# Kernel tuning notes

Hardware: AMD Instinct MI355X
Metric: run time of the kernel (lower is better)

Reference implementation:

```python
import jax, jax.numpy as jnp
import numpy as np

D = 1024

def setup_inputs() -> dict:
    key = jax.random.key(0)
    k1, k2, k3, k4, k5 = jax.random.split(key, 5)
    B, S = 128, 512
    seq_output = jax.random.normal(k1, (B, S, D), dtype=jnp.float32)
    mask = jax.random.randint(k2, (B, S), 0, 2) == 1  # True = masked position
    # ensure last position is never fully-masked pathological: fine either way
    scale1 = 1.0 / np.sqrt(D)
    W1 = jax.random.normal(k3, (D, D), dtype=jnp.float32) * scale1
    b1 = jnp.zeros((D,), dtype=jnp.float32)
    w2 = jax.random.normal(k4, (D,), dtype=jnp.float32) * scale1
    return {"seq_output": seq_output, "mask": mask, "W1": W1, "b1": b1, "w2": w2}

def reference(seq_output, mask, W1, b1, w2):
    # u_last: last timestep embedding
    u_last = seq_output[:, -1, :]                           # [B, D]
    # additive attention MLP: Linear -> tanh -> Linear(D->1, no bias)
    h = jnp.tanh(jnp.einsum('bsd,de->bse', seq_output, W1) + b1)  # [B, S, D]
    scores = jnp.einsum('bsd,d->bs', h, w2)                 # [B, S]
    scores = jnp.where(mask, -1e9, scores)
    attn = jax.nn.softmax(scores, axis=-1)                  # [B, S]
    u_att = jnp.einsum('bs,bsd->bd', attn, seq_output)      # [B, D]
    return (u_last, u_att)
```

## Files before the change

### kernel.cpp

```cpp
#include <hip/hip_runtime.h>
#include <hip/hip_bf16.h>
#include <cstdint>
#include <cstddef>

#define BATCH 128
#define SEQ   512
#define DIM   1024
#define MROWS (BATCH * SEQ)
#define NT    32

typedef short short8 __attribute__((ext_vector_type(8)));
typedef __bf16 bf16x8 __attribute__((ext_vector_type(8)));
typedef float f32x4 __attribute__((ext_vector_type(4)));

template <typename VA> struct other_frag { using type = bf16x8; };
template <> struct other_frag<bf16x8> { using type = short8; };

template <typename VA>
__device__ __forceinline__ auto try_mfma(VA a, VA b, f32x4 c, int)
    -> decltype(__builtin_amdgcn_mfma_f32_16x16x32_bf16(a, b, c, 0, 0, 0)) {
  return __builtin_amdgcn_mfma_f32_16x16x32_bf16(a, b, c, 0, 0, 0);
}
template <typename VA>
__device__ __forceinline__ f32x4 try_mfma(VA a, VA b, f32x4 c, long) {
  using O = typename other_frag<VA>::type;
  O a2 = __builtin_bit_cast(O, a);
  O b2 = __builtin_bit_cast(O, b);
  return __builtin_amdgcn_mfma_f32_16x16x32_bf16(a2, b2, c, 0, 0, 0);
}
__device__ __forceinline__ f32x4 mfma_bf16(short8 a, short8 b, f32x4 c) {
  return try_mfma(a, b, c, 0);
}

__device__ __forceinline__ unsigned short f32_to_bf16(float f) {
  union { float f; uint32_t u; } v; v.f = f;
  uint32_t u = v.u;
  u += 0x7FFFu + ((u >> 16) & 1u);
  return (unsigned short)(u >> 16);
}

__device__ __forceinline__ float bf16_to_f32(unsigned short u) {
  union { uint32_t u; float f; } v; v.u = ((uint32_t)u) << 16; return v.f;
}

__device__ __forceinline__ void gload_lds16(const void* g, void* l) {
  __builtin_amdgcn_global_load_lds(
      (__attribute__((address_space(1))) void*)g,
      (__attribute__((address_space(3))) void*)l,
      16, 0, 0);
}

__device__ __forceinline__ float fast_tanh(float x) {
  x = fminf(fmaxf(x, -15.0f), 15.0f);
  float e = __expf(2.0f * x);
  return (e - 1.0f) / (e + 1.0f);
}

__global__ __launch_bounds__(256) void cast_x_kernel(const float* __restrict__ X,
                                                     unsigned short* __restrict__ Xb) {
  const int total8 = MROWS * DIM / 8;
  int idx = blockIdx.x * 256 + threadIdx.x;
  const int stride = 2048 * 256;
  for (int i = idx; i < total8; i += stride) {
    const f32x4* p = (const f32x4*)X + (size_t)i * 2;
    f32x4 a = p[0];
    f32x4 b = p[1];
    short8 o;
    o[0] = (short)f32_to_bf16(a[0]); o[1] = (short)f32_to_bf16(a[1]);
    o[2] = (short)f32_to_bf16(a[2]); o[3] = (short)f32_to_bf16(a[3]);
    o[4] = (short)f32_to_bf16(b[0]); o[5] = (short)f32_to_bf16(b[1]);
    o[6] = (short)f32_to_bf16(b[2]); o[7] = (short)f32_to_bf16(b[3]);
    *((short8*)Xb + i) = o;
  }
}

__global__ __launch_bounds__(256) void w1t_kernel(const float* __restrict__ W1,
                                                  unsigned short* __restrict__ W1t) {
  __shared__ float tile[64][65];
  int bx = blockIdx.x & 15;
  int by = blockIdx.x >> 4;
  int t = threadIdx.x;
  int c = t & 63, r0 = t >> 6;
#pragma unroll
  for (int i = 0; i < 16; i++) {
    int r = i * 4 + r0;
    tile[r][c] = W1[(size_t)(by * 64 + r) * DIM + bx * 64 + c];
  }
  __syncthreads();
#pragma unroll
  for (int i = 0; i < 16; i++) {
    int r = i * 4 + r0;
    W1t[(size_t)(bx * 64 + r) * DIM + by * 64 + c] = f32_to_bf16(tile[c][r]);
  }
}

__global__ __launch_bounds__(256) void ulast_kernel(const float* __restrict__ X,
                                                    float* __restrict__ u_last) {
  int i = blockIdx.x * 256 + threadIdx.x;
  int b = i >> 8;
  int d4 = i & 255;
  ((f32x4*)u_last)[i] = ((const f32x4*)X)[((size_t)b * SEQ + (SEQ - 1)) * 256 + d4];
}

__global__ __launch_bounds__(512, 2) void gemm_score_kernel(
    const unsigned short* __restrict__ Xb,
    const unsigned short* __restrict__ W1t,
    const float* __restrict__ b1,
    const float* __restrict__ w2,
    float* __restrict__ scores) {
  __shared__ __align__(16) char lds[131072];

  const int tid = threadIdx.x;
  const int lane = tid & 63;
  const int w = tid >> 6;
  const int wr = w >> 2, wc = w & 3;

  const int bx = blockIdx.x;
  const int swz = (bx & 7) * 128 + (bx >> 3);
  const int m0 = (swz >> 2) * 256;
  const int n0 = (swz & 3) * 256;

  const unsigned short *a0Src, *a1Src, *b0Src, *b1Src;
  {
    int sc0 = w * 64 + lane;
    int sr0 = sc0 >> 3, j0 = (sc0 & 7) ^ (sr0 & 7);
    int row0 = sr0 * 2 + (j0 >> 2), c40 = j0 & 3;
    a0Src = Xb  + (size_t)(m0 + row0) * DIM + c40 * 8;
    b0Src = W1t + (size_t)(n0 + row0) * DIM + c40 * 8;
    int sc1 = (8 + w) * 64 + lane;
    int sr1 = sc1 >> 3, j1 = (sc1 & 7) ^ (sr1 & 7);
    int row1 = sr1 * 2 + (j1 >> 2), c41 = j1 & 3;
    a1Src = Xb  + (size_t)(m0 + row1) * DIM + c41 * 8;
    b1Src = W1t + (size_t)(n0 + row1) * DIM + c41 * 8;
  }
  const int dst0 = w * 1024;
  const int dst1 = (8 + w) * 1024;

  int aOff[8];
#pragma unroll
  for (int mi = 0; mi < 8; mi++) {
    int row = wr * 128 + mi * 16 + (lane & 15);
    int srow = row >> 1;
    int ic = ((row & 1) * 4 + (lane >> 4)) ^ (srow & 7);
    aOff[mi] = srow * 128 + ic * 16;
  }
  int bOff[4];
#pragma unroll
  for (int ni = 0; ni < 4; ni++) {
    int row = wc * 64 + ni * 16 + (lane & 15);
    int srow = row >> 1;
    int ic = ((row & 1) * 4 + (lane >> 4)) ^ (srow & 7);
    bOff[ni] = 65536 + srow * 128 + ic * 16;
  }

  f32x4 acc[8][4];
#pragma unroll
  for (int mi = 0; mi < 8; mi++)
#pragma unroll
    for (int ni = 0; ni < 4; ni++)
      acc[mi][ni] = (f32x4){0.f, 0.f, 0.f, 0.f};

#define STAGE(S) do {                                                   \
    const int bufS_ = ((S) & 3) * 16384;                                \
    const int ktS_ = (S) * 32;                                          \
    gload_lds16(a0Src + ktS_, lds + bufS_ + dst0);                      \
    gload_lds16(a1Src + ktS_, lds + bufS_ + dst1);                      \
    gload_lds16(b0Src + ktS_, lds + 65536 + bufS_ + dst0);              \
    gload_lds16(b1Src + ktS_, lds + 65536 + bufS_ + dst1);              \
  } while (0)

#define KITER(S, VMSTR) do {                                            \
    asm volatile("s_waitcnt vmcnt(" VMSTR ")" ::: "memory");            \
    __builtin_amdgcn_s_barrier();                                       \
    __builtin_amdgcn_sched_barrier(0);                                  \
    if ((S) + 3 < NT) STAGE((S) + 3);                                   \
    const int buf_ = ((S) & 3) * 16384;                                 \
    short8 af[8], bfv[4];                                               \
    _Pragma("unroll")                                                   \
    for (int mi = 0; mi < 8; mi++)                                      \
      af[mi] = *(const short8*)(lds + buf_ + aOff[mi]);                 \
    _Pragma("unroll")                                                   \
    for (int ni = 0; ni < 4; ni++)                                      \
      bfv[ni] = *(const short8*)(lds + buf_ + bOff[ni]);                \
    __builtin_amdgcn_s_setprio(1);                                      \
    _Pragma("unroll")                                                   \
    for (int mi = 0; mi < 8; mi++)                                      \
      _Pragma("unroll")                                                 \
      for (int ni = 0; ni < 4; ni++)                                    \
        acc[mi][ni] = mfma_bf16(af[mi], bfv[ni], acc[mi][ni]);          \
    __builtin_amdgcn_s_setprio(0);                                      \
  } while (0)

  STAGE(0); STAGE(1); STAGE(2);

  for (int s = 0; s < NT - 2; ++s) KITER(s, "8");
  KITER(NT - 2, "4");
  KITER(NT - 1, "0");

#undef STAGE
#undef KITER

  const int cg = lane >> 4;
  const int cl = lane & 15;
#pragma unroll
  for (int mi = 0; mi < 8; mi++) {
    float p0 = 0.f, p1 = 0.f, p2 = 0.f, p3 = 0.f;
#pragma unroll
    for (int ni = 0; ni < 4; ni++) {
      int col = n0 + wc * 64 + ni * 16 + cl;
      float w2v = w2[col];
      float b1v = b1[col];
      p0 += fast_tanh(acc[mi][ni][0] + b1v) * w2v;
      p1 += fast_tanh(acc[mi][ni][1] + b1v) * w2v;
      p2 += fast_tanh(acc[mi][ni][2] + b1v) * w2v;
      p3 += fast_tanh(acc[mi][ni][3] + b1v) * w2v;
    }
#pragma unroll
    for (int off = 1; off < 16; off <<= 1) {
      p0 += __shfl_xor(p0, off);
      p1 += __shfl_xor(p1, off);
      p2 += __shfl_xor(p2, off);
      p3 += __shfl_xor(p3, off);
    }
    if (cl == 0) {
      int row = m0 + wr * 128 + mi * 16 + cg * 4;
      atomicAdd(&scores[row + 0], p0);
      atomicAdd(&scores[row + 1], p1);
      atomicAdd(&scores[row + 2], p2);
      atomicAdd(&scores[row + 3], p3);
    }
  }
}

__global__ __launch_bounds__(256) void attn_uatt_kernel(
    const unsigned short* __restrict__ Xb,
    const float* __restrict__ scores,
    const int* __restrict__ mask,
    float* __restrict__ u_att) {
  const int b = blockIdx.x;
  const int half = blockIdx.y;
  const int tid = threadIdx.x;
  const int lane = tid & 63;
  const int wave = tid >> 6;

  __shared__ float attn[SEQ];
  __shared__ float rbuf[4];
  __shared__ float part[3][64 * 9];

  float s0 = scores[(size_t)b * SEQ + tid];
  float s1 = scores[(size_t)b * SEQ + 256 + tid];
  if (mask[(size_t)b * SEQ + tid]) s0 = -1000000000.0f;
  if (mask[(size_t)b * SEQ + 256 + tid]) s1 = -1000000000.0f;

  float mx = fmaxf(s0, s1);
#pragma unroll
  for (int off = 1; off < 64; off <<= 1) mx = fmaxf(mx, __shfl_xor(mx, off));
  if (lane == 0) rbuf[wave] = mx;
  __syncthreads();
  mx = fmaxf(fmaxf(rbuf[0], rbuf[1]), fmaxf(rbuf[2], rbuf[3]));

  float p0 = expf(s0 - mx), p1 = expf(s1 - mx);
  float sm = p0 + p1;
#pragma unroll
  for (int off = 1; off < 64; off <<= 1) sm += __shfl_xor(sm, off);
  __syncthreads();
  if (lane == 0) rbuf[wave] = sm;
  __syncthreads();
  sm = rbuf[0] + rbuf[1] + rbuf[2] + rbuf[3];
  float inv = 1.0f / sm;
  attn[tid] = p0 * inv;
  attn[tid + 256] = p1 * inv;
  __syncthreads();

  const int col = tid & 63;
  const int sh = tid >> 6;
  const short8* Xp = (const short8*)Xb + (size_t)b * SEQ * (DIM / 8) + half * 64 + col;
  float a[8] = {0.f, 0.f, 0.f, 0.f, 0.f, 0.f, 0.f, 0.f};
  for (int s = sh * 128; s < sh * 128 + 128; s++) {
    short8 v = Xp[(size_t)s * (DIM / 8)];
    float wgt = attn[s];
#pragma unroll
    for (int j = 0; j < 8; j++)
      a[j] += wgt * bf16_to_f32((unsigned short)v[j]);
  }
  if (sh) {
#pragma unroll
    for (int j = 0; j < 8; j++) part[sh - 1][col * 9 + j] = a[j];
  }
  __syncthreads();
  if (sh == 0) {
#pragma unroll
    for (int j = 0; j < 8; j++)
      a[j] += part[0][col * 9 + j] + part[1][col * 9 + j] + part[2][col * 9 + j];
    f32x4 lo = {a[0], a[1], a[2], a[3]};
    f32x4 hi = {a[4], a[5], a[6], a[7]};
    f32x4* dst = (f32x4*)(u_att + (size_t)b * DIM + half * 512 + col * 8);
    dst[0] = lo;
    dst[1] = hi;
  }
}

extern "C" void kernel_launch(void* const* d_in, const int* in_sizes, int n_in,
                              void* d_out, int out_size, void* d_ws, size_t ws_size,
                              hipStream_t stream) {
  const float* X    = (const float*)d_in[0];
  const int*   mask = (const int*)d_in[1];
  const float* W1   = (const float*)d_in[2];
  const float* b1   = (const float*)d_in[3];
  const float* w2   = (const float*)d_in[4];

  float* out    = (float*)d_out;
  float* u_last = out;
  float* u_att  = out + BATCH * DIM;

  char* ws = (char*)d_ws;
  unsigned short* Xb  = (unsigned short*)ws;
  unsigned short* W1t = (unsigned short*)(ws + (size_t)MROWS * DIM * 2);
  float* scores = (float*)(ws + (size_t)MROWS * DIM * 2 + (size_t)DIM * DIM * 2);

  hipMemsetAsync(scores, 0, MROWS * sizeof(float), stream);
  hipLaunchKernelGGL(cast_x_kernel, dim3(2048), dim3(256), 0, stream, X, Xb);
  hipLaunchKernelGGL(w1t_kernel, dim3(256), dim3(256), 0, stream, W1, W1t);
  hipLaunchKernelGGL(ulast_kernel, dim3(128), dim3(256), 0, stream, X, u_last);
  hipLaunchKernelGGL(gemm_score_kernel, dim3(1024), dim3(512), 0, stream,
                     Xb, W1t, b1, w2, scores);
  hipLaunchKernelGGL(attn_uatt_kernel, dim3(128, 2), dim3(256), 0, stream,
                     Xb, scores, mask, u_att);
}
```

Baseline: 266.6 us.

## Fuse fp32-to-bf16 cast of X into GEMM A-tile loading and drop cast kernel

The separate cast kernel that wrote a bf16 copy of X is removed. The GEMM now loads fp32 A tiles into registers, packs them to bf16 and writes them to LDS through a restructured double-buffered pipeline, with B going to a triple buffer and each K step split into two half-M MFMA phases. The attention kernel reads fp32 X directly and also writes u_last, which drops the ulast kernel. This removes a full write and re-read of the 128 MB bf16 copy, but the GEMM now reads twice as many A bytes (fp32) per tile, repeated across the four N-tile blocks, and adds more barriers per iteration.

```diff
diff --git a/kernel.cpp b/kernel.cpp
--- a/kernel.cpp
+++ b/kernel.cpp
@@ -39,8 +39,13 @@
   return (unsigned short)(u >> 16);
 }
 
-__device__ __forceinline__ float bf16_to_f32(unsigned short u) {
-  union { uint32_t u; float f; } v; v.u = ((uint32_t)u) << 16; return v.f;
+__device__ __forceinline__ short8 pack8(f32x4 a, f32x4 b) {
+  short8 o;
+  o[0] = (short)f32_to_bf16(a[0]); o[1] = (short)f32_to_bf16(a[1]);
+  o[2] = (short)f32_to_bf16(a[2]); o[3] = (short)f32_to_bf16(a[3]);
+  o[4] = (short)f32_to_bf16(b[0]); o[5] = (short)f32_to_bf16(b[1]);
+  o[6] = (short)f32_to_bf16(b[2]); o[7] = (short)f32_to_bf16(b[3]);
+  return o;
 }
 
 __device__ __forceinline__ void gload_lds16(const void* g, void* l) {
@@ -54,24 +59,6 @@
   x = fminf(fmaxf(x, -15.0f), 15.0f);
   float e = __expf(2.0f * x);
   return (e - 1.0f) / (e + 1.0f);
-}
-
-__global__ __launch_bounds__(256) void cast_x_kernel(const float* __restrict__ X,
-                                                     unsigned short* __restrict__ Xb) {
-  const int total8 = MROWS * DIM / 8;
-  int idx = blockIdx.x * 256 + threadIdx.x;
-  const int stride = 2048 * 256;
-  for (int i = idx; i < total8; i += stride) {
-    const f32x4* p = (const f32x4*)X + (size_t)i * 2;
-    f32x4 a = p[0];
-    f32x4 b = p[1];
-    short8 o;
-    o[0] = (short)f32_to_bf16(a[0]); o[1] = (short)f32_to_bf16(a[1]);
-    o[2] = (short)f32_to_bf16(a[2]); o[3] = (short)f32_to_bf16(a[3]);
-    o[4] = (short)f32_to_bf16(b[0]); o[5] = (short)f32_to_bf16(b[1]);
-    o[6] = (short)f32_to_bf16(b[2]); o[7] = (short)f32_to_bf16(b[3]);
-    *((short8*)Xb + i) = o;
-  }
 }
 
 __global__ __launch_bounds__(256) void w1t_kernel(const float* __restrict__ W1,
@@ -94,21 +81,13 @@
   }
 }
 
-__global__ __launch_bounds__(256) void ulast_kernel(const float* __restrict__ X,
-                                                    float* __restrict__ u_last) {
-  int i = blockIdx.x * 256 + threadIdx.x;
-  int b = i >> 8;
-  int d4 = i & 255;
-  ((f32x4*)u_last)[i] = ((const f32x4*)X)[((size_t)b * SEQ + (SEQ - 1)) * 256 + d4];
-}
-
 __global__ __launch_bounds__(512, 2) void gemm_score_kernel(
-    const unsigned short* __restrict__ Xb,
+    const float* __restrict__ Xf,
     const unsigned short* __restrict__ W1t,
     const float* __restrict__ b1,
     const float* __restrict__ w2,
     float* __restrict__ scores) {
-  __shared__ __align__(16) char lds[131072];
+  __shared__ __align__(16) char lds[81920];
 
   const int tid = threadIdx.x;
   const int lane = tid & 63;
@@ -120,37 +99,36 @@
   const int m0 = (swz >> 2) * 256;
   const int n0 = (swz & 3) * 256;
 
-  const unsigned short *a0Src, *a1Src, *b0Src, *b1Src;
+  const int j_sw = (tid & 7) ^ ((tid >> 3) & 7);
+  const int ar0 = (tid >> 3) * 2 + (j_sw >> 2);
+  const float* aS0 = Xf + (size_t)(m0 + ar0) * DIM + (j_sw & 3) * 8;
+
+  const unsigned short *b0Src, *b1Src;
   {
-    int sc0 = w * 64 + lane;
-    int sr0 = sc0 >> 3, j0 = (sc0 & 7) ^ (sr0 & 7);
+    int sr0 = tid >> 3, j0 = (tid & 7) ^ (sr0 & 7);
     int row0 = sr0 * 2 + (j0 >> 2), c40 = j0 & 3;
-    a0Src = Xb  + (size_t)(m0 + row0) * DIM + c40 * 8;
     b0Src = W1t + (size_t)(n0 + row0) * DIM + c40 * 8;
-    int sc1 = (8 + w) * 64 + lane;
+    int sc1 = 512 + tid;
     int sr1 = sc1 >> 3, j1 = (sc1 & 7) ^ (sr1 & 7);
     int row1 = sr1 * 2 + (j1 >> 2), c41 = j1 & 3;
-    a1Src = Xb  + (size_t)(m0 + row1) * DIM + c41 * 8;
     b1Src = W1t + (size_t)(n0 + row1) * DIM + c41 * 8;
   }
-  const int dst0 = w * 1024;
-  const int dst1 = (8 + w) * 1024;
-
-  int aOff[8];
-#pragma unroll
-  for (int mi = 0; mi < 8; mi++) {
+
+  int aOffL[4];
+#pragma unroll
+  for (int mi = 0; mi < 4; mi++) {
     int row = wr * 128 + mi * 16 + (lane & 15);
-    int srow = row >> 1;
-    int ic = ((row & 1) * 4 + (lane >> 4)) ^ (srow & 7);
-    aOff[mi] = srow * 128 + ic * 16;
-  }
-  int bOff[4];
+    int sr = row >> 1;
+    int j = ((row & 1) * 4 + (lane >> 4)) ^ (sr & 7);
+    aOffL[mi] = sr * 128 + j * 16;
+  }
+  int bOffL[4];
 #pragma unroll
   for (int ni = 0; ni < 4; ni++) {
     int row = wc * 64 + ni * 16 + (lane & 15);
-    int srow = row >> 1;
-    int ic = ((row & 1) * 4 + (lane >> 4)) ^ (srow & 7);
-    bOff[ni] = 65536 + srow * 128 + ic * 16;
+    int sr = row >> 1;
+    int j = ((row & 1) * 4 + (lane >> 4)) ^ (sr & 7);
+    bOffL[ni] = sr * 128 + j * 16;
   }
 
   f32x4 acc[8][4];
@@ -160,45 +138,113 @@
     for (int ni = 0; ni < 4; ni++)
       acc[mi][ni] = (f32x4){0.f, 0.f, 0.f, 0.f};
 
-#define STAGE(S) do {                                                   \
-    const int bufS_ = ((S) & 3) * 16384;                                \
-    const int ktS_ = (S) * 32;                                          \
-    gload_lds16(a0Src + ktS_, lds + bufS_ + dst0);                      \
-    gload_lds16(a1Src + ktS_, lds + bufS_ + dst1);                      \
-    gload_lds16(b0Src + ktS_, lds + 65536 + bufS_ + dst0);              \
-    gload_lds16(b1Src + ktS_, lds + 65536 + bufS_ + dst1);              \
+  f32x4 rA0[4], rA1[4];
+  short8 af[4], bf[4];
+
+#define LOAD_A(SET, T) do {                                              \
+    const float* aP_ = aS0 + (T) * 32;                                   \
+    SET[0] = *(const f32x4*)(aP_);                                       \
+    SET[1] = *(const f32x4*)(aP_ + 4);                                   \
+    SET[2] = *(const f32x4*)(aP_ + (size_t)128 * DIM);                   \
+    SET[3] = *(const f32x4*)(aP_ + (size_t)128 * DIM + 4);               \
   } while (0)
 
-#define KITER(S, VMSTR) do {                                            \
-    asm volatile("s_waitcnt vmcnt(" VMSTR ")" ::: "memory");            \
-    __builtin_amdgcn_s_barrier();                                       \
-    __builtin_amdgcn_sched_barrier(0);                                  \
-    if ((S) + 3 < NT) STAGE((S) + 3);                                   \
-    const int buf_ = ((S) & 3) * 16384;                                 \
-    short8 af[8], bfv[4];                                               \
-    _Pragma("unroll")                                                   \
-    for (int mi = 0; mi < 8; mi++)                                      \
-      af[mi] = *(const short8*)(lds + buf_ + aOff[mi]);                 \
-    _Pragma("unroll")                                                   \
-    for (int ni = 0; ni < 4; ni++)                                      \
-      bfv[ni] = *(const short8*)(lds + buf_ + bOff[ni]);                \
-    __builtin_amdgcn_s_setprio(1);                                      \
-    _Pragma("unroll")                                                   \
-    for (int mi = 0; mi < 8; mi++)                                      \
-      _Pragma("unroll")                                                 \
-      for (int ni = 0; ni < 4; ni++)                                    \
-        acc[mi][ni] = mfma_bf16(af[mi], bfv[ni], acc[mi][ni]);          \
-    __builtin_amdgcn_s_setprio(0);                                      \
+  LOAD_A(rA0, 0);
+  __builtin_amdgcn_sched_barrier(0);
+  gload_lds16(b0Src, lds + 32768 + w * 1024);
+  gload_lds16(b1Src, lds + 32768 + 8192 + w * 1024);
+  __builtin_amdgcn_sched_barrier(0);
+  LOAD_A(rA1, 1);
+  __builtin_amdgcn_sched_barrier(0);
+  gload_lds16(b0Src + 32, lds + 32768 + 16384 + w * 1024);
+  gload_lds16(b1Src + 32, lds + 32768 + 16384 + 8192 + w * 1024);
+  __builtin_amdgcn_sched_barrier(0);
+  asm volatile("s_waitcnt vmcnt(8)" ::: "memory");
+  {
+    short8 w0 = pack8(rA0[0], rA0[1]);
+    short8 w1 = pack8(rA0[2], rA0[3]);
+    char* wd = lds + tid * 16;
+    *(short8*)wd = w0;
+    *(short8*)(wd + 8192) = w1;
+  }
+  asm volatile("s_waitcnt vmcnt(6)" ::: "memory");
+  asm volatile("s_waitcnt lgkmcnt(0)" ::: "memory");
+  __builtin_amdgcn_sched_barrier(0);
+  __builtin_amdgcn_s_barrier();
+
+#define BODY(S, ISET, WSET, PF, DOWR, VMSTR) do {                        \
+                                               \
+    if (PF) {                                                            \
+      LOAD_A(ISET, (S) + 2);                                             \
+      gload_lds16(b0Src + ((S) + 2) * 32,                                \
+                  lds + 32768 + (((S) + 2) % 3) * 16384 + w * 1024);     \
+    }                                                                    \
+    __builtin_amdgcn_sched_barrier(0);                                   \
+    {                                                                    \
+      const char* bA_ = lds + ((S) & 1) * 16384;                         \
+      const char* bB_ = lds + 32768 + ((S) % 3) * 16384;                 \
+      af[0] = *(const short8*)(bA_ + aOffL[0]);                          \
+      af[1] = *(const short8*)(bA_ + aOffL[1]);                          \
+      af[2] = *(const short8*)(bA_ + aOffL[2]);                          \
+      af[3] = *(const short8*)(bA_ + aOffL[3]);                          \
+      bf[0] = *(const short8*)(bB_ + bOffL[0]);                          \
+      bf[1] = *(const short8*)(bB_ + bOffL[1]);                          \
+      bf[2] = *(const short8*)(bB_ + bOffL[2]);                          \
+      bf[3] = *(const short8*)(bB_ + bOffL[3]);                          \
+    }                                                                    \
+    __builtin_amdgcn_sched_barrier(0);                                   \
+    __builtin_amdgcn_s_barrier();                                        \
+    __builtin_amdgcn_s_setprio(1);                                       \
+    _Pragma("unroll")                                                    \
+    for (int mi = 0; mi < 4; mi++)                                       \
+      _Pragma("unroll")                                                  \
+      for (int ni = 0; ni < 4; ni++)                                     \
+        acc[mi][ni] = mfma_bf16(af[mi], bf[ni], acc[mi][ni]);            \
+    __builtin_amdgcn_s_setprio(0);                                       \
+    __builtin_amdgcn_s_barrier();                                        \
+                                               \
+    asm volatile("s_waitcnt vmcnt(" VMSTR ")" ::: "memory");             \
+    __builtin_amdgcn_sched_barrier(0);                                   \
+    if (DOWR) {                                                          \
+      short8 w0_ = pack8(WSET[0], WSET[1]);                              \
+      short8 w1_ = pack8(WSET[2], WSET[3]);                              \
+      char* wd_ = lds + (((S) + 1) & 1) * 16384 + tid * 16;              \
+      *(short8*)wd_ = w0_;                                               \
+      *(short8*)(wd_ + 8192) = w1_;                                      \
+    }                                                                    \
+    if (PF)                                                              \
+      gload_lds16(b1Src + ((S) + 2) * 32,                                \
+                  lds + 32768 + (((S) + 2) % 3) * 16384 + 8192 + w * 1024); \
+    __builtin_amdgcn_sched_barrier(0);                                   \
+    {                                                                    \
+      const char* bA_ = lds + ((S) & 1) * 16384;                         \
+      af[0] = *(const short8*)(bA_ + aOffL[0] + 4096);                   \
+      af[1] = *(const short8*)(bA_ + aOffL[1] + 4096);                   \
+      af[2] = *(const short8*)(bA_ + aOffL[2] + 4096);                   \
+      af[3] = *(const short8*)(bA_ + aOffL[3] + 4096);                   \
+    }                                                                    \
+    __builtin_amdgcn_sched_barrier(0);                                   \
+    __builtin_amdgcn_s_barrier();                                        \
+    __builtin_amdgcn_s_setprio(1);                                       \
+    _Pragma("unroll")                                                    \
+    for (int mi = 0; mi < 4; mi++)                                       \
+      _Pragma("unroll")                                                  \
+      for (int ni = 0; ni < 4; ni++)                                     \
+        acc[mi + 4][ni] = mfma_bf16(af[mi], bf[ni], acc[mi + 4][ni]);    \
+    __builtin_amdgcn_s_setprio(0);                                       \
+    __builtin_amdgcn_s_barrier();                                        \
   } while (0)
 
-  STAGE(0); STAGE(1); STAGE(2);
-
-  for (int s = 0; s < NT - 2; ++s) KITER(s, "8");
-  KITER(NT - 2, "4");
-  KITER(NT - 1, "0");
-
-#undef STAGE
-#undef KITER
+  for (int t = 0; t < 15; ++t) {
+    const int S0 = 2 * t;
+    BODY(S0, rA0, rA1, 1, 1, "5");
+    BODY(S0 + 1, rA1, rA0, 1, 1, "5");
+  }
+  BODY(30, rA0, rA1, 0, 1, "0");
+  BODY(31, rA1, rA0, 0, 0, "0");
+
+#undef BODY
+#undef LOAD_A
 
   const int cg = lane >> 4;
   const int cl = lane & 15;
@@ -233,10 +279,11 @@
 }
 
 __global__ __launch_bounds__(256) void attn_uatt_kernel(
-    const unsigned short* __restrict__ Xb,
+    const float* __restrict__ X,
     const float* __restrict__ scores,
     const int* __restrict__ mask,
-    float* __restrict__ u_att) {
+    float* __restrict__ u_att,
+    float* __restrict__ u_last) {
   const int b = blockIdx.x;
   const int half = blockIdx.y;
   const int tid = threadIdx.x;
@@ -272,31 +319,37 @@
   attn[tid + 256] = p1 * inv;
   __syncthreads();
 
+  if (tid < 128) {
+    ((f32x4*)u_last)[(size_t)b * 256 + half * 128 + tid] =
+        ((const f32x4*)X)[((size_t)b * SEQ + (SEQ - 1)) * 256 + half * 128 + tid];
+  }
+
   const int col = tid & 63;
   const int sh = tid >> 6;
-  const short8* Xp = (const short8*)Xb + (size_t)b * SEQ * (DIM / 8) + half * 64 + col;
-  float a[8] = {0.f, 0.f, 0.f, 0.f, 0.f, 0.f, 0.f, 0.f};
+  const f32x4* Xp = (const f32x4*)X + (size_t)b * SEQ * 256 + half * 128 + col * 2;
+  f32x4 a0 = {0.f, 0.f, 0.f, 0.f}, a1 = {0.f, 0.f, 0.f, 0.f};
   for (int s = sh * 128; s < sh * 128 + 128; s++) {
-    short8 v = Xp[(size_t)s * (DIM / 8)];
     float wgt = attn[s];
-#pragma unroll
-    for (int j = 0; j < 8; j++)
-      a[j] += wgt * bf16_to_f32((unsigned short)v[j]);
+    a0 += wgt * Xp[(size_t)s * 256];
+    a1 += wgt * Xp[(size_t)s * 256 + 1];
   }
   if (sh) {
 #pragma unroll
-    for (int j = 0; j < 8; j++) part[sh - 1][col * 9 + j] = a[j];
+    for (int j = 0; j < 4; j++) part[sh - 1][col * 9 + j] = a0[j];
+#pragma unroll
+    for (int j = 0; j < 4; j++) part[sh - 1][col * 9 + 4 + j] = a1[j];
   }
   __syncthreads();
   if (sh == 0) {
 #pragma unroll
-    for (int j = 0; j < 8; j++)
-      a[j] += part[0][col * 9 + j] + part[1][col * 9 + j] + part[2][col * 9 + j];
-    f32x4 lo = {a[0], a[1], a[2], a[3]};
-    f32x4 hi = {a[4], a[5], a[6], a[7]};
+    for (int j = 0; j < 4; j++)
+      a0[j] += part[0][col * 9 + j] + part[1][col * 9 + j] + part[2][col * 9 + j];
+#pragma unroll
+    for (int j = 0; j < 4; j++)
+      a1[j] += part[0][col * 9 + 4 + j] + part[1][col * 9 + 4 + j] + part[2][col * 9 + 4 + j];
     f32x4* dst = (f32x4*)(u_att + (size_t)b * DIM + half * 512 + col * 8);
-    dst[0] = lo;
-    dst[1] = hi;
+    dst[0] = a0;
+    dst[1] = a1;
   }
 }
 
@@ -314,16 +367,13 @@
   float* u_att  = out + BATCH * DIM;
 
   char* ws = (char*)d_ws;
-  unsigned short* Xb  = (unsigned short*)ws;
-  unsigned short* W1t = (unsigned short*)(ws + (size_t)MROWS * DIM * 2);
-  float* scores = (float*)(ws + (size_t)MROWS * DIM * 2 + (size_t)DIM * DIM * 2);
+  unsigned short* W1t = (unsigned short*)ws;
+  float* scores = (float*)(ws + (size_t)DIM * DIM * 2);
 
   hipMemsetAsync(scores, 0, MROWS * sizeof(float), stream);
-  hipLaunchKernelGGL(cast_x_kernel, dim3(2048), dim3(256), 0, stream, X, Xb);
   hipLaunchKernelGGL(w1t_kernel, dim3(256), dim3(256), 0, stream, W1, W1t);
-  hipLaunchKernelGGL(ulast_kernel, dim3(128), dim3(256), 0, stream, X, u_last);
   hipLaunchKernelGGL(gemm_score_kernel, dim3(1024), dim3(512), 0, stream,
-                     Xb, W1t, b1, w2, scores);
+                     X, W1t, b1, w2, scores);
   hipLaunchKernelGGL(attn_uatt_kernel, dim3(128, 2), dim3(256), 0, stream,
-                     Xb, scores, mask, u_att);
-}
+                     X, scores, mask, u_att, u_last);
+}
```

New measurement: 256.0 us. -4.0%, faster.

## Split each K-iteration into two half-phases interleaving loads with MFMA

Applied to the files above, without the earlier changes.

Each K-step of the GEMM now runs in two phases. The first issues the A-tile global-to-LDS prefetch, reads half of the A fragments plus the B fragments, and runs half of the MFMAs. The second issues the B prefetch, reads the other half of A, and runs the remaining MFMAs. The aim is to cut fragment register pressure and spread memory issue across the MFMA work, ping-pong style. It adds three extra workgroup barriers per iteration, which could cost synchronisation time.

```diff
diff --git a/kernel.cpp b/kernel.cpp
--- a/kernel.cpp
+++ b/kernel.cpp
@@ -160,11 +160,18 @@
     for (int ni = 0; ni < 4; ni++)
       acc[mi][ni] = (f32x4){0.f, 0.f, 0.f, 0.f};
 
-#define STAGE(S) do {                                                   \
+  short8 af[4], bfv[4];
+
+#define STAGE_A(S) do {                                                 \
     const int bufS_ = ((S) & 3) * 16384;                                \
     const int ktS_ = (S) * 32;                                          \
     gload_lds16(a0Src + ktS_, lds + bufS_ + dst0);                      \
     gload_lds16(a1Src + ktS_, lds + bufS_ + dst1);                      \
+  } while (0)
+
+#define STAGE_B(S) do {                                                 \
+    const int bufS_ = ((S) & 3) * 16384;                                \
+    const int ktS_ = (S) * 32;                                          \
     gload_lds16(b0Src + ktS_, lds + 65536 + bufS_ + dst0);              \
     gload_lds16(b1Src + ktS_, lds + 65536 + bufS_ + dst1);              \
   } while (0)
@@ -173,31 +180,50 @@
     asm volatile("s_waitcnt vmcnt(" VMSTR ")" ::: "memory");            \
     __builtin_amdgcn_s_barrier();                                       \
     __builtin_amdgcn_sched_barrier(0);                                  \
-    if ((S) + 3 < NT) STAGE((S) + 3);                                   \
     const int buf_ = ((S) & 3) * 16384;                                 \
-    short8 af[8], bfv[4];                                               \
-    _Pragma("unroll")                                                   \
-    for (int mi = 0; mi < 8; mi++)                                      \
+                                                 \
+    if ((S) + 3 < NT) STAGE_A((S) + 3);                                 \
+    _Pragma("unroll")                                                   \
+    for (int mi = 0; mi < 4; mi++)                                      \
       af[mi] = *(const short8*)(lds + buf_ + aOff[mi]);                 \
     _Pragma("unroll")                                                   \
     for (int ni = 0; ni < 4; ni++)                                      \
       bfv[ni] = *(const short8*)(lds + buf_ + bOff[ni]);                \
+    __builtin_amdgcn_s_barrier();                                       \
     __builtin_amdgcn_s_setprio(1);                                      \
     _Pragma("unroll")                                                   \
-    for (int mi = 0; mi < 8; mi++)                                      \
+    for (int mi = 0; mi < 4; mi++)                                      \
       _Pragma("unroll")                                                 \
       for (int ni = 0; ni < 4; ni++)                                    \
         acc[mi][ni] = mfma_bf16(af[mi], bfv[ni], acc[mi][ni]);          \
     __builtin_amdgcn_s_setprio(0);                                      \
+    __builtin_amdgcn_s_barrier();                                       \
+    __builtin_amdgcn_sched_barrier(0);                                  \
+                                                 \
+    if ((S) + 3 < NT) STAGE_B((S) + 3);                                 \
+    _Pragma("unroll")                                                   \
+    for (int mi = 0; mi < 4; mi++)                                      \
+      af[mi] = *(const short8*)(lds + buf_ + aOff[mi + 4]);             \
+    __builtin_amdgcn_s_barrier();                                       \
+    __builtin_amdgcn_s_setprio(1);                                      \
+    _Pragma("unroll")                                                   \
+    for (int mi = 0; mi < 4; mi++)                                      \
+      _Pragma("unroll")                                                 \
+      for (int ni = 0; ni < 4; ni++)                                    \
+        acc[mi + 4][ni] = mfma_bf16(af[mi], bfv[ni], acc[mi + 4][ni]);  \
+    __builtin_amdgcn_s_setprio(0);                                      \
   } while (0)
 
-  STAGE(0); STAGE(1); STAGE(2);
+  STAGE_A(0); STAGE_B(0);
+  STAGE_A(1); STAGE_B(1);
+  STAGE_A(2); STAGE_B(2);
 
   for (int s = 0; s < NT - 2; ++s) KITER(s, "8");
   KITER(NT - 2, "4");
   KITER(NT - 1, "0");
 
-#undef STAGE
+#undef STAGE_A
+#undef STAGE_B
 #undef KITER
 
   const int cg = lane >> 4;
```

New measurement: 267.8 us. Within noise of the previous version (+0.5%).

## Switch GEMM to 32x32x16 MFMA tiles and fold u_last copy into cast kernel

Applied to the files above, without the earlier changes.

The main GEMM moves from 16x16x32 bf16 MFMA to 32x32x16 MFMA. LDS fragment offsets, the accumulator layout and the tanh/w2 epilogue reduction are reworked to match the 32x32 output layout. Each wave now issues fewer, larger MFMAs and fewer LDS fragment reads per K-step. The separate u_last gather kernel is removed, and the cast kernel writes the last-timestep rows while it converts X, saving one launch. The epilogue now does a wider shuffle reduction over 16 values per lane, which may raise register pressure.

```diff
diff --git a/kernel.cpp b/kernel.cpp
--- a/kernel.cpp
+++ b/kernel.cpp
@@ -12,24 +12,25 @@
 typedef short short8 __attribute__((ext_vector_type(8)));
 typedef __bf16 bf16x8 __attribute__((ext_vector_type(8)));
 typedef float f32x4 __attribute__((ext_vector_type(4)));
+typedef float f32x16 __attribute__((ext_vector_type(16)));
 
 template <typename VA> struct other_frag { using type = bf16x8; };
 template <> struct other_frag<bf16x8> { using type = short8; };
 
 template <typename VA>
-__device__ __forceinline__ auto try_mfma(VA a, VA b, f32x4 c, int)
-    -> decltype(__builtin_amdgcn_mfma_f32_16x16x32_bf16(a, b, c, 0, 0, 0)) {
-  return __builtin_amdgcn_mfma_f32_16x16x32_bf16(a, b, c, 0, 0, 0);
+__device__ __forceinline__ auto try_mfma32(VA a, VA b, f32x16 c, int)
+    -> decltype(__builtin_amdgcn_mfma_f32_32x32x16_bf16(a, b, c, 0, 0, 0)) {
+  return __builtin_amdgcn_mfma_f32_32x32x16_bf16(a, b, c, 0, 0, 0);
 }
 template <typename VA>
-__device__ __forceinline__ f32x4 try_mfma(VA a, VA b, f32x4 c, long) {
+__device__ __forceinline__ f32x16 try_mfma32(VA a, VA b, f32x16 c, long) {
   using O = typename other_frag<VA>::type;
   O a2 = __builtin_bit_cast(O, a);
   O b2 = __builtin_bit_cast(O, b);
-  return __builtin_amdgcn_mfma_f32_16x16x32_bf16(a2, b2, c, 0, 0, 0);
-}
-__device__ __forceinline__ f32x4 mfma_bf16(short8 a, short8 b, f32x4 c) {
-  return try_mfma(a, b, c, 0);
+  return __builtin_amdgcn_mfma_f32_32x32x16_bf16(a2, b2, c, 0, 0, 0);
+}
+__device__ __forceinline__ f32x16 mfma32_bf16(short8 a, short8 b, f32x16 c) {
+  return try_mfma32(a, b, c, 0);
 }
 
 __device__ __forceinline__ unsigned short f32_to_bf16(float f) {
@@ -57,7 +58,8 @@
 }
 
 __global__ __launch_bounds__(256) void cast_x_kernel(const float* __restrict__ X,
-                                                     unsigned short* __restrict__ Xb) {
+                                                     unsigned short* __restrict__ Xb,
+                                                     float* __restrict__ u_last) {
   const int total8 = MROWS * DIM / 8;
   int idx = blockIdx.x * 256 + threadIdx.x;
   const int stride = 2048 * 256;
@@ -71,6 +73,13 @@
     o[4] = (short)f32_to_bf16(b[0]); o[5] = (short)f32_to_bf16(b[1]);
     o[6] = (short)f32_to_bf16(b[2]); o[7] = (short)f32_to_bf16(b[3]);
     *((short8*)Xb + i) = o;
+    int row = i >> 7;
+    if ((row & (SEQ - 1)) == SEQ - 1) {
+      int g = i & 127;
+      f32x4* dst = (f32x4*)(u_last + (size_t)(row >> 9) * DIM + g * 8);
+      dst[0] = a;
+      dst[1] = b;
+    }
   }
 }
 
@@ -92,14 +101,6 @@
     int r = i * 4 + r0;
     W1t[(size_t)(bx * 64 + r) * DIM + by * 64 + c] = f32_to_bf16(tile[c][r]);
   }
-}
-
-__global__ __launch_bounds__(256) void ulast_kernel(const float* __restrict__ X,
-                                                    float* __restrict__ u_last) {
-  int i = blockIdx.x * 256 + threadIdx.x;
-  int b = i >> 8;
-  int d4 = i & 255;
-  ((f32x4*)u_last)[i] = ((const f32x4*)X)[((size_t)b * SEQ + (SEQ - 1)) * 256 + d4];
 }
 
 __global__ __launch_bounds__(512, 2) void gemm_score_kernel(
@@ -136,29 +137,37 @@
   const int dst0 = w * 1024;
   const int dst1 = (8 + w) * 1024;
 
-  int aOff[8];
-#pragma unroll
-  for (int mi = 0; mi < 8; mi++) {
-    int row = wr * 128 + mi * 16 + (lane & 15);
+  int aOff[4][2];
+#pragma unroll
+  for (int mi = 0; mi < 4; mi++) {
+    int row = wr * 128 + mi * 32 + (lane & 31);
     int srow = row >> 1;
-    int ic = ((row & 1) * 4 + (lane >> 4)) ^ (srow & 7);
-    aOff[mi] = srow * 128 + ic * 16;
-  }
-  int bOff[4];
-#pragma unroll
-  for (int ni = 0; ni < 4; ni++) {
-    int row = wc * 64 + ni * 16 + (lane & 15);
+#pragma unroll
+    for (int kk = 0; kk < 2; kk++) {
+      int ic = ((row & 1) * 4 + kk * 2 + (lane >> 5)) ^ (srow & 7);
+      aOff[mi][kk] = srow * 128 + ic * 16;
+    }
+  }
+  int bOff[2][2];
+#pragma unroll
+  for (int ni = 0; ni < 2; ni++) {
+    int row = wc * 64 + ni * 32 + (lane & 31);
     int srow = row >> 1;
-    int ic = ((row & 1) * 4 + (lane >> 4)) ^ (srow & 7);
-    bOff[ni] = 65536 + srow * 128 + ic * 16;
-  }
-
-  f32x4 acc[8][4];
-#pragma unroll
-  for (int mi = 0; mi < 8; mi++)
-#pragma unroll
-    for (int ni = 0; ni < 4; ni++)
-      acc[mi][ni] = (f32x4){0.f, 0.f, 0.f, 0.f};
+#pragma unroll
+    for (int kk = 0; kk < 2; kk++) {
+      int ic = ((row & 1) * 4 + kk * 2 + (lane >> 5)) ^ (srow & 7);
+      bOff[ni][kk] = 65536 + srow * 128 + ic * 16;
+    }
+  }
+
+  f32x16 acc[4][2];
+#pragma unroll
+  for (int mi = 0; mi < 4; mi++)
+#pragma unroll
+    for (int ni = 0; ni < 2; ni++)
+      acc[mi][ni] = (f32x16)(0.f);
+
+  short8 af[4][2], bfv[2][2];
 
 #define STAGE(S) do {                                                   \
     const int bufS_ = ((S) & 3) * 16384;                                \
@@ -175,19 +184,24 @@
     __builtin_amdgcn_sched_barrier(0);                                  \
     if ((S) + 3 < NT) STAGE((S) + 3);                                   \
     const int buf_ = ((S) & 3) * 16384;                                 \
-    short8 af[8], bfv[4];                                               \
     _Pragma("unroll")                                                   \
-    for (int mi = 0; mi < 8; mi++)                                      \
-      af[mi] = *(const short8*)(lds + buf_ + aOff[mi]);                 \
+    for (int mi = 0; mi < 4; mi++)                                      \
+      _Pragma("unroll")                                                 \
+      for (int kk = 0; kk < 2; kk++)                                    \
+        af[mi][kk] = *(const short8*)(lds + buf_ + aOff[mi][kk]);       \
     _Pragma("unroll")                                                   \
-    for (int ni = 0; ni < 4; ni++)                                      \
-      bfv[ni] = *(const short8*)(lds + buf_ + bOff[ni]);                \
+    for (int ni = 0; ni < 2; ni++)                                      \
+      _Pragma("unroll")                                                 \
+      for (int kk = 0; kk < 2; kk++)                                    \
+        bfv[ni][kk] = *(const short8*)(lds + buf_ + bOff[ni][kk]);      \
     __builtin_amdgcn_s_setprio(1);                                      \
     _Pragma("unroll")                                                   \
-    for (int mi = 0; mi < 8; mi++)                                      \
+    for (int kk = 0; kk < 2; kk++)                                      \
       _Pragma("unroll")                                                 \
-      for (int ni = 0; ni < 4; ni++)                                    \
-        acc[mi][ni] = mfma_bf16(af[mi], bfv[ni], acc[mi][ni]);          \
+      for (int mi = 0; mi < 4; mi++)                                    \
+        _Pragma("unroll")                                               \
+        for (int ni = 0; ni < 2; ni++)                                  \
+          acc[mi][ni] = mfma32_bf16(af[mi][kk], bfv[ni][kk], acc[mi][ni]); \
     __builtin_amdgcn_s_setprio(0);                                      \
   } while (0)
 
@@ -200,34 +214,35 @@
 #undef STAGE
 #undef KITER
 
-  const int cg = lane >> 4;
-  const int cl = lane & 15;
-#pragma unroll
-  for (int mi = 0; mi < 8; mi++) {
-    float p0 = 0.f, p1 = 0.f, p2 = 0.f, p3 = 0.f;
-#pragma unroll
-    for (int ni = 0; ni < 4; ni++) {
-      int col = n0 + wc * 64 + ni * 16 + cl;
+  const int colL = lane & 31;
+  const int hi = lane >> 5;
+#pragma unroll
+  for (int mi = 0; mi < 4; mi++) {
+    float p[16];
+#pragma unroll
+    for (int r = 0; r < 16; r++) p[r] = 0.f;
+#pragma unroll
+    for (int ni = 0; ni < 2; ni++) {
+      int col = n0 + wc * 64 + ni * 32 + colL;
       float w2v = w2[col];
       float b1v = b1[col];
-      p0 += fast_tanh(acc[mi][ni][0] + b1v) * w2v;
-      p1 += fast_tanh(acc[mi][ni][1] + b1v) * w2v;
-      p2 += fast_tanh(acc[mi][ni][2] + b1v) * w2v;
-      p3 += fast_tanh(acc[mi][ni][3] + b1v) * w2v;
-    }
-#pragma unroll
-    for (int off = 1; off < 16; off <<= 1) {
-      p0 += __shfl_xor(p0, off);
-      p1 += __shfl_xor(p1, off);
-      p2 += __shfl_xor(p2, off);
-      p3 += __shfl_xor(p3, off);
-    }
-    if (cl == 0) {
-      int row = m0 + wr * 128 + mi * 16 + cg * 4;
-      atomicAdd(&scores[row + 0], p0);
-      atomicAdd(&scores[row + 1], p1);
-      atomicAdd(&scores[row + 2], p2);
-      atomicAdd(&scores[row + 3], p3);
+#pragma unroll
+      for (int r = 0; r < 16; r++)
+        p[r] += fast_tanh(acc[mi][ni][r] + b1v) * w2v;
+    }
+#pragma unroll
+    for (int off = 1; off < 32; off <<= 1) {
+#pragma unroll
+      for (int r = 0; r < 16; r++)
+        p[r] += __shfl_xor(p[r], off);
+    }
+    if (colL == 0) {
+      int mbase = m0 + wr * 128 + mi * 32 + 4 * hi;
+#pragma unroll
+      for (int r = 0; r < 16; r++) {
+        int row = mbase + (r & 3) + 8 * (r >> 2);
+        atomicAdd(&scores[row], p[r]);
+      }
     }
   }
 }
@@ -293,10 +308,10 @@
     for (int j = 0; j < 8; j++)
       a[j] += part[0][col * 9 + j] + part[1][col * 9 + j] + part[2][col * 9 + j];
     f32x4 lo = {a[0], a[1], a[2], a[3]};
-    f32x4 hi = {a[4], a[5], a[6], a[7]};
+    f32x4 hi4 = {a[4], a[5], a[6], a[7]};
     f32x4* dst = (f32x4*)(u_att + (size_t)b * DIM + half * 512 + col * 8);
     dst[0] = lo;
-    dst[1] = hi;
+    dst[1] = hi4;
   }
 }
 
@@ -319,9 +334,8 @@
   float* scores = (float*)(ws + (size_t)MROWS * DIM * 2 + (size_t)DIM * DIM * 2);
 
   hipMemsetAsync(scores, 0, MROWS * sizeof(float), stream);
-  hipLaunchKernelGGL(cast_x_kernel, dim3(2048), dim3(256), 0, stream, X, Xb);
+  hipLaunchKernelGGL(cast_x_kernel, dim3(2048), dim3(256), 0, stream, X, Xb, u_last);
   hipLaunchKernelGGL(w1t_kernel, dim3(256), dim3(256), 0, stream, W1, W1t);
-  hipLaunchKernelGGL(ulast_kernel, dim3(128), dim3(256), 0, stream, X, u_last);
   hipLaunchKernelGGL(gemm_score_kernel, dim3(1024), dim3(512), 0, stream,
                      Xb, W1t, b1, w2, scores);
   hipLaunchKernelGGL(attn_uatt_kernel, dim3(128, 2), dim3(256), 0, stream,
```

Measured after the change: 354.5 us. 1.33x slower.
